# Optimization experiments

Measured on AMD Instinct MI355X. Metric: run time of the kernel, lower is better.

## Reference

```python
import jax, jax.numpy as jnp
import numpy as np

NUM_HEADS = 4
NUM_GROUPS = 8
EPS = 1e-5


def group_norm(x, w, b):
    # x: [B, C, H, W], 8 groups, per-channel affine
    B, C, H, W = x.shape
    g = x.reshape(B, NUM_GROUPS, C // NUM_GROUPS, H, W)
    mu = g.mean(axis=(2, 3, 4), keepdims=True)
    var = g.var(axis=(2, 3, 4), keepdims=True)
    g = (g - mu) * jax.lax.rsqrt(var + EPS)
    x = g.reshape(B, C, H, W)
    return x * w[None, :, None, None] + b[None, :, None, None]


def setup_inputs() -> dict:
    key = jax.random.key(0)
    ks = jax.random.split(key, 7)
    B, C, H, W = 16, 256, 32, 32
    x = jax.random.normal(ks[0], (B, C, H, W), dtype=jnp.float32)
    norm_w = jnp.ones((C,), jnp.float32)
    norm_b = jnp.zeros((C,), jnp.float32)
    # 1x1 convs == channel matmuls; fan-in scaled init
    qkv_w = jax.random.normal(ks[1], (3 * C, C), dtype=jnp.float32) / np.sqrt(C)
    qkv_b = jnp.zeros((3 * C,), jnp.float32)
    proj_w = jax.random.normal(ks[2], (C, C), dtype=jnp.float32) / np.sqrt(C)
    proj_b = jnp.zeros((C,), jnp.float32)
    return {"x": x, "norm_w": norm_w, "norm_b": norm_b,
            "qkv_w": qkv_w, "qkv_b": qkv_b,
            "proj_w": proj_w, "proj_b": proj_b}


def reference(x, norm_w, norm_b, qkv_w, qkv_b, proj_w, proj_b):
    B, C, H, W = x.shape
    nh = NUM_HEADS
    d = C // nh
    N = H * W

    h = group_norm(x, norm_w, norm_b)
    # 1x1 conv -> channel matmul: [B, 3C, H, W]
    qkv = jnp.einsum('oc,bchw->bohw', qkv_w, h) + qkv_b[None, :, None, None]
    qkv = qkv.reshape(B, 3, nh, d, N)
    q, k, v = qkv[:, 0], qkv[:, 1], qkv[:, 2]  # [B, nh, d, N]

    scale = d ** (-0.5)
    attn = jnp.einsum('bhcn,bhcm->bhnm', q, k) * scale  # [B, nh, N, N]
    attn = jax.nn.softmax(attn, axis=-1)
    out = jnp.einsum('bhnm,bhcm->bhcn', attn, v)  # [B, nh, d, N]
    out = out.reshape(B, C, H, W)
    out = jnp.einsum('oc,bchw->bohw', proj_w, out) + proj_b[None, :, None, None]
    return x + out
```

## Files before the change

### kernel.cpp

```cpp
#include <hip/hip_runtime.h>
#include <math.h>

#define BATCH 16
#define CH 256
#define NG 8
#define NH 4
#define HD 64
#define NN 1024
#define GSZ 32
#define GELEMS (GSZ * NN)

typedef __attribute__((ext_vector_type(8))) __bf16 bf16x8;
typedef __attribute__((ext_vector_type(4))) __bf16 bf16x4;
typedef __attribute__((ext_vector_type(4))) float f32x4;

__device__ __forceinline__ unsigned short f2b(float f) {
    union { __bf16 h; unsigned short u; } c; c.h = (__bf16)f; return c.u;
}

#define MFMA(a, b, c) __builtin_amdgcn_mfma_f32_16x16x32_bf16(a, b, c, 0, 0, 0)

__global__ __launch_bounds__(256) void prep_kernel(
    const float* __restrict__ x, const float* __restrict__ qkv_w,
    const float* __restrict__ proj_w, float* __restrict__ stats,
    unsigned short* __restrict__ wq, unsigned short* __restrict__ wp)
{
    int tid = threadIdx.x;
    if (blockIdx.x >= 128) {
        int t = (blockIdx.x - 128) * 256 + tid;
        const float* src; unsigned short* dst; size_t off;
        if (t < 24576) { src = qkv_w; dst = wq; off = (size_t)t * 8; }
        else           { src = proj_w; dst = wp; off = (size_t)(t - 24576) * 8; }
        const float4* s4 = (const float4*)(src + off);
        float4 a = s4[0], b = s4[1];
        bf16x8 pk;
        pk[0] = (__bf16)a.x; pk[1] = (__bf16)a.y; pk[2] = (__bf16)a.z; pk[3] = (__bf16)a.w;
        pk[4] = (__bf16)b.x; pk[5] = (__bf16)b.y; pk[6] = (__bf16)b.z; pk[7] = (__bf16)b.w;
        *(bf16x8*)(dst + off) = pk;
        return;
    }
    int b = blockIdx.x >> 3, g = blockIdx.x & 7;
    const float4* x4 = (const float4*)(x + ((size_t)b * CH + g * GSZ) * NN);
    float s = 0.f, ss = 0.f;
    #pragma unroll
    for (int i = 0; i < 32; ++i) {
        float4 v = x4[tid + i * 256];
        s  += v.x + v.y + v.z + v.w;
        ss += v.x * v.x + v.y * v.y + v.z * v.z + v.w * v.w;
    }
    #pragma unroll
    for (int off = 1; off < 64; off <<= 1) {
        s  += __shfl_xor(s, off);
        ss += __shfl_xor(ss, off);
    }
    __shared__ float red[8];
    int wave = tid >> 6, lane = tid & 63;
    if (lane == 0) { red[wave] = s; red[4 + wave] = ss; }
    __syncthreads();
    if (tid == 0) {
        float ts  = red[0] + red[1] + red[2] + red[3];
        float tss = red[4] + red[5] + red[6] + red[7];
        float mu  = ts * (1.f / GELEMS);
        float var = tss * (1.f / GELEMS) - mu * mu;
        stats[blockIdx.x * 2] = mu;
        stats[blockIdx.x * 2 + 1] = rsqrtf(var + 1e-5f);
    }
}

__global__ __launch_bounds__(256) void gn_apply_kernel(
    const float* __restrict__ x, const float* __restrict__ w,
    const float* __restrict__ bb, const float* __restrict__ stats,
    unsigned short* __restrict__ hT)
{
    __shared__ float Ts[64][68];
    __shared__ float wcp[256], bcp[256];
    const int b = blockIdx.y, n0 = blockIdx.x * 64;
    const int tid = threadIdx.x;
    {
        int c = tid, g = c >> 5;
        float mu = stats[(b * 8 + g) * 2], rs = stats[(b * 8 + g) * 2 + 1];
        float wc = w[c] * rs;
        wcp[c] = wc; bcp[c] = bb[c] - mu * wc;
    }
    __syncthreads();
    const float* xb = x + (size_t)b * CH * NN;
    const int c_l = tid >> 2, nq = tid & 3;
    const int n_l = tid >> 2, cq = tid & 3;
    for (int cb = 0; cb < 4; ++cb) {
        #pragma unroll
        for (int i = 0; i < 4; ++i)
            *(float4*)&Ts[c_l][nq * 4 + i * 16] =
                *(const float4*)(xb + (size_t)(cb * 64 + c_l) * NN + n0 + nq * 4 + i * 16);
        __syncthreads();
        #pragma unroll
        for (int s = 0; s < 2; ++s) {
            int cbase = cq * 16 + s * 8;
            bf16x8 pk;
            #pragma unroll
            for (int j = 0; j < 8; ++j) {
                int c = cb * 64 + cbase + j;
                pk[j] = (__bf16)(Ts[cbase + j][n_l] * wcp[c] + bcp[c]);
            }
            *(bf16x8*)(hT + ((size_t)b * NN + n0 + n_l) * CH + cb * 64 + cbase) = pk;
        }
        __syncthreads();
    }
}

template <int KIND>
__global__ __launch_bounds__(256) void gemm_kernel(
    const unsigned short* __restrict__ AT,
    const unsigned short* __restrict__ Wb,
    const float* __restrict__ bias,
    unsigned short* __restrict__ outT, unsigned short* __restrict__ outV,
    const float* __restrict__ res, float* __restrict__ out)
{
    __shared__ __align__(16) unsigned short Ws[64][136];
    __shared__ __align__(16) unsigned short Hs[64][136];
    const int b = blockIdx.z, o0 = blockIdx.y * 64, n0 = blockIdx.x * 64;
    const int tid = threadIdx.x;
    const int lane = tid & 63, wv = tid >> 6;
    const int l = lane & 15, quad = lane >> 4;
    const int iw = wv & 1, jw = wv >> 1;
    const bool qk_mode = (KIND == 0) && (blockIdx.y < 8);
    const int r4 = tid >> 2, c4 = tid & 3;

    f32x4 acc[2][2] = {};
    for (int st = 0; st < 2; ++st) {
        const int cc0 = st * 128;
        #pragma unroll
        for (int i = 0; i < 4; ++i) {
            int ch = c4 + i * 4;
            *(bf16x8*)&Ws[r4][ch * 8] =
                *(const bf16x8*)(Wb + (size_t)(o0 + r4) * CH + cc0 + ch * 8);
            *(bf16x8*)&Hs[r4][ch * 8] =
                *(const bf16x8*)(AT + ((size_t)b * NN + n0 + r4) * CH + cc0 + ch * 8);
        }
        __syncthreads();
        #pragma unroll
        for (int kt = 0; kt < 4; ++kt) {
            bf16x8 af[2], bf[2];
            #pragma unroll
            for (int i = 0; i < 2; ++i)
                af[i] = *(const bf16x8*)&Hs[iw * 32 + i * 16 + l][kt * 32 + quad * 8];
            #pragma unroll
            for (int j = 0; j < 2; ++j)
                bf[j] = *(const bf16x8*)&Ws[jw * 32 + j * 16 + l][kt * 32 + quad * 8];
            #pragma unroll
            for (int i = 0; i < 2; ++i)
                #pragma unroll
                for (int j = 0; j < 2; ++j)
                    acc[i][j] = qk_mode ? MFMA(af[i], bf[j], acc[i][j])
                                        : MFMA(bf[j], af[i], acc[i][j]);
        }
        __syncthreads();
    }

    #pragma unroll
    for (int i = 0; i < 2; ++i)
        #pragma unroll
        for (int j = 0; j < 2; ++j) {
            if (qk_mode) {
                int o = o0 + jw * 32 + j * 16 + l;
                float bs = bias[o];
                #pragma unroll
                for (int r = 0; r < 4; ++r) {
                    int n = n0 + iw * 32 + i * 16 + quad * 4 + r;
                    outT[((size_t)b * NN + n) * 512 + o] = f2b(acc[i][j][r] + bs);
                }
            } else {
                int o = o0 + jw * 32 + j * 16 + quad * 4;
                int n = n0 + iw * 32 + i * 16 + l;
                #pragma unroll
                for (int r = 0; r < 4; ++r) {
                    float v = acc[i][j][r] + bias[o + r];
                    if (KIND == 0)
                        outV[((size_t)b * CH + (o + r - 512)) * NN + n] = f2b(v);
                    else {
                        size_t idx = ((size_t)b * CH + o + r) * NN + n;
                        out[idx] = v + res[idx];
                    }
                }
            }
        }
}

__global__ __launch_bounds__(256) void attn_kernel(
    const unsigned short* __restrict__ qkvT,
    const unsigned short* __restrict__ vbuf,
    unsigned short* __restrict__ ctxT)
{
    __shared__ __align__(16) unsigned short Ps[4][32][40];
    __shared__ float Ored[2][32][64];
    __shared__ float Lred[2][2][32];
    const int id = blockIdx.x;
    const int bh = id & 63, nt = id >> 6;
    const int b = bh >> 2, hh = bh & 3;
    const int n0 = nt * 64;
    const int tid = threadIdx.x;
    const int lane = tid & 63, w = tid >> 6;
    const int l = lane & 15, quad = lane >> 4;
    const int qx = w & 1, ky = w >> 1;
    const float KL2E = 0.125f * 1.44269504f;

    bf16x8 qf[2][2];
    {
        const unsigned short* qp = qkvT + ((size_t)b * NN + n0 + 32 * qx + l) * 512 + hh * 64;
        #pragma unroll
        for (int ns = 0; ns < 2; ++ns)
            #pragma unroll
            for (int kt = 0; kt < 2; ++kt)
                qf[ns][kt] = *(const bf16x8*)(qp + (size_t)ns * 16 * 512 + kt * 32 + quad * 8);
    }
    const unsigned short* kp = qkvT + ((size_t)b * NN + 32 * ky + l) * 512 + 256 + hh * 64
                               + quad * 8;
    const unsigned short* vp = vbuf + ((size_t)b * CH + hh * 64 + l) * NN + 32 * ky + quad * 8;

    float l_w[2] = {0.f, 0.f};
    f32x4 oacc[2][4] = {};

    #pragma unroll 2
    for (int mt = 0; mt < 16; ++mt) {
        const int m0 = mt * 64;
        bf16x8 kf[2][2], vf[4];
        #pragma unroll
        for (int mt2 = 0; mt2 < 2; ++mt2)
            #pragma unroll
            for (int kt = 0; kt < 2; ++kt)
                kf[mt2][kt] = *(const bf16x8*)(kp + (size_t)(m0 + 16 * mt2) * 512 + kt * 32);
        #pragma unroll
        for (int ct = 0; ct < 4; ++ct)
            vf[ct] = *(const bf16x8*)(vp + (size_t)(16 * ct) * NN + m0);

        f32x4 sacc[2][2] = {};
        #pragma unroll
        for (int kt = 0; kt < 2; ++kt)
            #pragma unroll
            for (int mt2 = 0; mt2 < 2; ++mt2)
                #pragma unroll
                for (int ns = 0; ns < 2; ++ns)
                    sacc[mt2][ns] = MFMA(kf[mt2][kt], qf[ns][kt], sacc[mt2][ns]);

        #pragma unroll
        for (int ns = 0; ns < 2; ++ns)
            #pragma unroll
            for (int mt2 = 0; mt2 < 2; ++mt2) {
                bf16x4 pk;
                #pragma unroll
                for (int r = 0; r < 4; ++r) {
                    float p = exp2f(sacc[mt2][ns][r] * KL2E);
                    l_w[ns] += p;
                    pk[r] = (__bf16)p;
                }
                *(bf16x4*)&Ps[w][ns * 16 + l][mt2 * 16 + quad * 4] = pk;
            }

        #pragma unroll
        for (int ns = 0; ns < 2; ++ns) {
            bf16x8 pa = *(const bf16x8*)&Ps[w][ns * 16 + l][quad * 8];
            #pragma unroll
            for (int ct = 0; ct < 4; ++ct)
                oacc[ns][ct] = MFMA(pa, vf[ct], oacc[ns][ct]);
        }
    }

    #pragma unroll
    for (int ns = 0; ns < 2; ++ns) {
        l_w[ns] += __shfl_xor(l_w[ns], 16);
        l_w[ns] += __shfl_xor(l_w[ns], 32);
    }
    if (ky == 1) {
        #pragma unroll
        for (int ns = 0; ns < 2; ++ns) {
            if (quad == 0) Lred[0][qx][ns * 16 + l] = l_w[ns];
            #pragma unroll
            for (int ct = 0; ct < 4; ++ct)
                #pragma unroll
                for (int r = 0; r < 4; ++r)
                    Ored[qx][ns * 16 + quad * 4 + r][ct * 16 + l] = oacc[ns][ct][r];
        }
    }
    __syncthreads();
    if (ky == 0) {
        #pragma unroll
        for (int ns = 0; ns < 2; ++ns)
            if (quad == 0)
                Lred[1][qx][ns * 16 + l] = l_w[ns] + Lred[0][qx][ns * 16 + l];
        unsigned short* cb = ctxT + ((size_t)b * NN + n0 + 32 * qx) * CH + hh * 64;
        #pragma unroll
        for (int ns = 0; ns < 2; ++ns) {
            float inv[4];
            #pragma unroll
            for (int r = 0; r < 4; ++r)
                inv[r] = 1.f / Lred[1][qx][ns * 16 + quad * 4 + r];
            #pragma unroll
            for (int ct = 0; ct < 4; ++ct)
                #pragma unroll
                for (int r = 0; r < 4; ++r) {
                    float o = oacc[ns][ct][r] +
                              Ored[qx][ns * 16 + quad * 4 + r][ct * 16 + l];
                    cb[(size_t)(ns * 16 + quad * 4 + r) * CH + ct * 16 + l] = f2b(o * inv[r]);
                }
        }
    }
}

extern "C" void kernel_launch(void* const* d_in, const int* in_sizes, int n_in,
                              void* d_out, int out_size, void* d_ws, size_t ws_size,
                              hipStream_t stream)
{
    const float* x      = (const float*)d_in[0];
    const float* norm_w = (const float*)d_in[1];
    const float* norm_b = (const float*)d_in[2];
    const float* qkv_w  = (const float*)d_in[3];
    const float* qkv_b  = (const float*)d_in[4];
    const float* proj_w = (const float*)d_in[5];
    const float* proj_b = (const float*)d_in[6];
    float* out = (float*)d_out;

    unsigned short* hT   = (unsigned short*)d_ws;
    unsigned short* qkvT = hT   + (size_t)BATCH * NN * CH;
    unsigned short* vbuf = qkvT + (size_t)BATCH * NN * 512;
    unsigned short* ctxT = vbuf + (size_t)BATCH * CH * NN;
    unsigned short* wq   = ctxT + (size_t)BATCH * NN * CH;
    unsigned short* wp   = wq + (size_t)768 * CH;
    float* stats         = (float*)(wp + (size_t)CH * CH);

    prep_kernel<<<dim3(256), 256, 0, stream>>>(x, qkv_w, proj_w, stats, wq, wp);
    gn_apply_kernel<<<dim3(16, BATCH), 256, 0, stream>>>(x, norm_w, norm_b, stats, hT);
    gemm_kernel<0><<<dim3(NN / 64, 12, BATCH), 256, 0, stream>>>(
        hT, wq, qkv_b, qkvT, vbuf, nullptr, nullptr);
    attn_kernel<<<dim3(1024), 256, 0, stream>>>(qkvT, vbuf, ctxT);
    gemm_kernel<1><<<dim3(NN / 64, 4, BATCH), 256, 0, stream>>>(
        ctxT, wp, proj_b, nullptr, nullptr, x, out);
}
```

Baseline: 179.7 us.

## Stage K/V tiles in double-buffered swizzled LDS and drop P round-trip via fp16 MFMA

The attention kernel now cooperatively loads each 64-key K and V tile into a double-buffered, XOR-swizzled LDS buffer, prefetching the next tile into registers while computing the current one. P is no longer written to LDS and reread. Instead the exp values feed a 16x16x16 fp16 MFMA directly as the B operand, with V stored as fp16 so the accumulator layout matches. The epilogue reuses the KV buffer for the cross-wave reduction and writes bf16x4 vectors. This cuts redundant global loads and LDS traffic but adds a barrier per iteration and changes P/V precision to fp16.

```diff
diff --git a/kernel.cpp b/kernel.cpp
--- a/kernel.cpp
+++ b/kernel.cpp
@@ -12,13 +12,18 @@
 
 typedef __attribute__((ext_vector_type(8))) __bf16 bf16x8;
 typedef __attribute__((ext_vector_type(4))) __bf16 bf16x4;
+typedef __attribute__((ext_vector_type(4))) _Float16 f16x4;
 typedef __attribute__((ext_vector_type(4))) float f32x4;
 
 __device__ __forceinline__ unsigned short f2b(float f) {
     union { __bf16 h; unsigned short u; } c; c.h = (__bf16)f; return c.u;
 }
+__device__ __forceinline__ unsigned short f2h(float f) {
+    union { _Float16 h; unsigned short u; } c; c.h = (_Float16)f; return c.u;
+}
 
 #define MFMA(a, b, c) __builtin_amdgcn_mfma_f32_16x16x32_bf16(a, b, c, 0, 0, 0)
+#define MFMA16(a, b, c) __builtin_amdgcn_mfma_f32_16x16x16f16(a, b, c, 0, 0, 0)
 
 __global__ __launch_bounds__(256) void prep_kernel(
     const float* __restrict__ x, const float* __restrict__ qkv_w,
@@ -175,7 +180,7 @@
                 for (int r = 0; r < 4; ++r) {
                     float v = acc[i][j][r] + bias[o + r];
                     if (KIND == 0)
-                        outV[((size_t)b * CH + (o + r - 512)) * NN + n] = f2b(v);
+                        outV[((size_t)b * CH + (o + r - 512)) * NN + n] = f2h(v);
                     else {
                         size_t idx = ((size_t)b * CH + o + r) * NN + n;
                         out[idx] = v + res[idx];
@@ -185,14 +190,13 @@
         }
 }
 
-__global__ __launch_bounds__(256) void attn_kernel(
+__global__ __launch_bounds__(256, 3) void attn_kernel(
     const unsigned short* __restrict__ qkvT,
     const unsigned short* __restrict__ vbuf,
     unsigned short* __restrict__ ctxT)
 {
-    __shared__ __align__(16) unsigned short Ps[4][32][40];
-    __shared__ float Ored[2][32][64];
-    __shared__ float Lred[2][2][32];
+    __shared__ __align__(16) unsigned short KV[2][8192];
+    __shared__ float Lred[2][32];
     const int id = blockIdx.x;
     const int bh = id & 63, nt = id >> 6;
     const int b = bh >> 2, hh = bh & 3;
@@ -202,6 +206,7 @@
     const int l = lane & 15, quad = lane >> 4;
     const int qx = w & 1, ky = w >> 1;
     const float KL2E = 0.125f * 1.44269504f;
+    const int r4 = tid >> 2, c4 = tid & 3;
 
     bf16x8 qf[2][2];
     {
@@ -212,25 +217,43 @@
             for (int kt = 0; kt < 2; ++kt)
                 qf[ns][kt] = *(const bf16x8*)(qp + (size_t)ns * 16 * 512 + kt * 32 + quad * 8);
     }
-    const unsigned short* kp = qkvT + ((size_t)b * NN + 32 * ky + l) * 512 + 256 + hh * 64
-                               + quad * 8;
-    const unsigned short* vp = vbuf + ((size_t)b * CH + hh * 64 + l) * NN + 32 * ky + quad * 8;
+
+    const unsigned short* gk = qkvT + ((size_t)b * NN + r4) * 512 + 256 + hh * 64;
+    const unsigned short* gv = vbuf + ((size_t)b * CH + hh * 64 + r4) * NN;
+    const int p0 = (c4 ^ (r4 & 7)) * 8, p1 = ((c4 + 4) ^ (r4 & 7)) * 8;
+
+    bf16x8 kpre0, kpre1, vpre0, vpre1;
+    kpre0 = *(const bf16x8*)(gk + c4 * 8);
+    kpre1 = *(const bf16x8*)(gk + (c4 + 4) * 8);
+    vpre0 = *(const bf16x8*)(gv + c4 * 8);
+    vpre1 = *(const bf16x8*)(gv + (c4 + 4) * 8);
+    *(bf16x8*)&KV[0][r4 * 64 + p0] = kpre0;
+    *(bf16x8*)&KV[0][r4 * 64 + p1] = kpre1;
+    *(bf16x8*)&KV[0][4096 + r4 * 64 + p0] = vpre0;
+    *(bf16x8*)&KV[0][4096 + r4 * 64 + p1] = vpre1;
+    __syncthreads();
 
     float l_w[2] = {0.f, 0.f};
     f32x4 oacc[2][4] = {};
 
-    #pragma unroll 2
     for (int mt = 0; mt < 16; ++mt) {
-        const int m0 = mt * 64;
-        bf16x8 kf[2][2], vf[4];
+        const int cur = mt & 1;
+        if (mt < 15) {
+            const unsigned short* gk1 = gk + (size_t)(mt + 1) * 64 * 512;
+            const unsigned short* gv1 = gv + (mt + 1) * 64;
+            kpre0 = *(const bf16x8*)(gk1 + c4 * 8);
+            kpre1 = *(const bf16x8*)(gk1 + (c4 + 4) * 8);
+            vpre0 = *(const bf16x8*)(gv1 + c4 * 8);
+            vpre1 = *(const bf16x8*)(gv1 + (c4 + 4) * 8);
+        }
+
+        bf16x8 kf[2][2];
         #pragma unroll
         for (int mt2 = 0; mt2 < 2; ++mt2)
             #pragma unroll
             for (int kt = 0; kt < 2; ++kt)
-                kf[mt2][kt] = *(const bf16x8*)(kp + (size_t)(m0 + 16 * mt2) * 512 + kt * 32);
-        #pragma unroll
-        for (int ct = 0; ct < 4; ++ct)
-            vf[ct] = *(const bf16x8*)(vp + (size_t)(16 * ct) * NN + m0);
+                kf[mt2][kt] = *(const bf16x8*)
+                    &KV[cur][(32 * ky + 16 * mt2 + l) * 64 + (((kt * 4 + quad) ^ (l & 7)) * 8)];
 
         f32x4 sacc[2][2] = {};
         #pragma unroll
@@ -241,26 +264,38 @@
                 for (int ns = 0; ns < 2; ++ns)
                     sacc[mt2][ns] = MFMA(kf[mt2][kt], qf[ns][kt], sacc[mt2][ns]);
 
-        #pragma unroll
-        for (int ns = 0; ns < 2; ++ns)
-            #pragma unroll
-            for (int mt2 = 0; mt2 < 2; ++mt2) {
-                bf16x4 pk;
+        f16x4 pf[2][2];
+        #pragma unroll
+        for (int mt2 = 0; mt2 < 2; ++mt2)
+            #pragma unroll
+            for (int ns = 0; ns < 2; ++ns)
                 #pragma unroll
                 for (int r = 0; r < 4; ++r) {
                     float p = exp2f(sacc[mt2][ns][r] * KL2E);
                     l_w[ns] += p;
-                    pk[r] = (__bf16)p;
+                    pf[mt2][ns][r] = (_Float16)p;
                 }
-                *(bf16x4*)&Ps[w][ns * 16 + l][mt2 * 16 + quad * 4] = pk;
+
+        #pragma unroll
+        for (int mt2 = 0; mt2 < 2; ++mt2) {
+            const int q8 = 4 * ky + 2 * mt2 + (quad >> 1);
+            const int vo = ((q8 ^ (l & 7)) * 8) + (quad & 1) * 4;
+            #pragma unroll
+            for (int ct = 0; ct < 4; ++ct) {
+                f16x4 va = *(const f16x4*)&KV[cur][4096 + (16 * ct + l) * 64 + vo];
+                #pragma unroll
+                for (int ns = 0; ns < 2; ++ns)
+                    oacc[ns][ct] = MFMA16(va, pf[mt2][ns], oacc[ns][ct]);
             }
-
-        #pragma unroll
-        for (int ns = 0; ns < 2; ++ns) {
-            bf16x8 pa = *(const bf16x8*)&Ps[w][ns * 16 + l][quad * 8];
-            #pragma unroll
-            for (int ct = 0; ct < 4; ++ct)
-                oacc[ns][ct] = MFMA(pa, vf[ct], oacc[ns][ct]);
+        }
+
+        if (mt < 15) {
+            const int nxt = cur ^ 1;
+            *(bf16x8*)&KV[nxt][r4 * 64 + p0] = kpre0;
+            *(bf16x8*)&KV[nxt][r4 * 64 + p1] = kpre1;
+            *(bf16x8*)&KV[nxt][4096 + r4 * 64 + p0] = vpre0;
+            *(bf16x8*)&KV[nxt][4096 + r4 * 64 + p1] = vpre1;
+            __syncthreads();
         }
     }
 
@@ -269,38 +304,34 @@
         l_w[ns] += __shfl_xor(l_w[ns], 16);
         l_w[ns] += __shfl_xor(l_w[ns], 32);
     }
+    float* Ored = (float*)&KV[0][0];
     if (ky == 1) {
         #pragma unroll
         for (int ns = 0; ns < 2; ++ns) {
-            if (quad == 0) Lred[0][qx][ns * 16 + l] = l_w[ns];
+            if (quad == 0) Lred[qx][ns * 16 + l] = l_w[ns];
             #pragma unroll
             for (int ct = 0; ct < 4; ++ct)
                 #pragma unroll
                 for (int r = 0; r < 4; ++r)
-                    Ored[qx][ns * 16 + quad * 4 + r][ct * 16 + l] = oacc[ns][ct][r];
+                    Ored[qx * 2048 + (16 * ct + quad * 4 + r) * 32 + ns * 16 + l] =
+                        oacc[ns][ct][r];
         }
     }
     __syncthreads();
     if (ky == 0) {
-        #pragma unroll
-        for (int ns = 0; ns < 2; ++ns)
-            if (quad == 0)
-                Lred[1][qx][ns * 16 + l] = l_w[ns] + Lred[0][qx][ns * 16 + l];
         unsigned short* cb = ctxT + ((size_t)b * NN + n0 + 32 * qx) * CH + hh * 64;
         #pragma unroll
         for (int ns = 0; ns < 2; ++ns) {
-            float inv[4];
-            #pragma unroll
-            for (int r = 0; r < 4; ++r)
-                inv[r] = 1.f / Lred[1][qx][ns * 16 + quad * 4 + r];
-            #pragma unroll
-            for (int ct = 0; ct < 4; ++ct)
-                #pragma unroll
-                for (int r = 0; r < 4; ++r) {
-                    float o = oacc[ns][ct][r] +
-                              Ored[qx][ns * 16 + quad * 4 + r][ct * 16 + l];
-                    cb[(size_t)(ns * 16 + quad * 4 + r) * CH + ct * 16 + l] = f2b(o * inv[r]);
-                }
+            float inv = 1.f / (l_w[ns] + Lred[qx][ns * 16 + l]);
+            #pragma unroll
+            for (int ct = 0; ct < 4; ++ct) {
+                bf16x4 pk;
+                #pragma unroll
+                for (int r = 0; r < 4; ++r)
+                    pk[r] = (__bf16)((oacc[ns][ct][r] +
+                             Ored[qx * 2048 + (16 * ct + quad * 4 + r) * 32 + ns * 16 + l]) * inv);
+                *(bf16x4*)(cb + (size_t)(ns * 16 + l) * CH + 16 * ct + quad * 4) = pk;
+            }
         }
     }
 }
```

After: 147.9 us. 17.7% less time.
